# Kernel optimization log

Hardware: AMD Instinct MI355X
Metric: run time of the kernel (lower is better)

## Reference

```python
import jax, jax.numpy as jnp
import numpy as np

B = 2; QD = 128; H = QD; W = QD; NQ = QD * QD
EMBED = 256; HEADS = 8; POINTS = 4; D = EMBED // HEADS; FFN = 512


def setup_inputs() -> dict:
    key = jax.random.key(0)
    ks = jax.random.split(key, 16)
    s = 0.02
    rn = lambda k, shp: jax.random.normal(k, shp, jnp.float32) * s
    return {
        'q': jax.random.normal(ks[0], (B, NQ, EMBED), jnp.float32),
        'W_off': rn(ks[1], (EMBED, HEADS * POINTS * 2)),
        'b_off': rn(ks[2], (HEADS * POINTS * 2,)),
        'W_attn': rn(ks[3], (EMBED, HEADS * POINTS)),
        'b_attn': rn(ks[4], (HEADS * POINTS,)),
        'W_val': rn(ks[5], (EMBED, EMBED)),
        'b_val': rn(ks[6], (EMBED,)),
        'W_out': rn(ks[7], (EMBED, EMBED)),
        'b_out': rn(ks[8], (EMBED,)),
        'W1': rn(ks[9], (EMBED, FFN)),
        'b1': rn(ks[10], (FFN,)),
        'W2': rn(ks[11], (FFN, EMBED)),
        'b2': rn(ks[12], (EMBED,)),
        'gamma': jnp.ones((EMBED,), jnp.float32),
        'beta': jnp.zeros((EMBED,), jnp.float32),
    }


def _layernorm(x, g, b):
    m = x.mean(-1, keepdims=True)
    v = ((x - m) ** 2).mean(-1, keepdims=True)
    return (x - m) * jax.lax.rsqrt(v + 1e-5) * g + b


def _msda(q, W_off, b_off, W_attn, b_attn, W_val, b_val, W_out, b_out):
    # value projection; value == query here. (B, NQ, EMBED)
    value = q @ W_val + b_val
    v = value.reshape(B, NQ, HEADS, D).transpose(0, 2, 1, 3)  # (B, heads, Nv, D)

    off = (q @ W_off + b_off).reshape(B, NQ, HEADS, POINTS, 2)
    aw = jax.nn.softmax((q @ W_attn + b_attn).reshape(B, NQ, HEADS, POINTS), axis=-1)

    # reference points: torch.meshgrid(linspace, linspace, indexing='xy')
    lin = jnp.linspace(0.0, 1.0, QD)
    gx, gy = jnp.meshgrid(lin, lin, indexing='xy')
    ref = jnp.stack([gx, gy], -1).reshape(1, NQ, 1, 1, 2)

    # offset_normalizer = [W, H]; sampling locations in [0,1]
    loc = ref + off / jnp.array([W, H], jnp.float32)
    # grid_sample bilinear, align_corners=False: pixel = loc * size - 0.5
    px = (loc[..., 0] * W - 0.5).transpose(0, 2, 1, 3)  # (B, heads, NQ, P)
    py = (loc[..., 1] * H - 0.5).transpose(0, 2, 1, 3)

    x0 = jnp.floor(px)
    y0 = jnp.floor(py)
    sampled = jnp.zeros((B, HEADS, NQ, POINTS, D), jnp.float32)
    for dy in (0.0, 1.0):
        for dx in (0.0, 1.0):
            xi = x0 + dx
            yi = y0 + dy
            wgt = (1.0 - jnp.abs(px - xi)) * (1.0 - jnp.abs(py - yi))
            valid = ((xi >= 0) & (xi <= W - 1) & (yi >= 0) & (yi <= H - 1)).astype(jnp.float32)
            idx = (jnp.clip(yi, 0, H - 1).astype(jnp.int32) * W
                   + jnp.clip(xi, 0, W - 1).astype(jnp.int32))  # (B, heads, NQ, P)
            g = jnp.take_along_axis(v, idx.reshape(B, HEADS, NQ * POINTS, 1), axis=2)
            g = g.reshape(B, HEADS, NQ, POINTS, D)
            sampled = sampled + g * (wgt * valid)[..., None]

    awt = aw.transpose(0, 2, 1, 3)  # (B, heads, NQ, P)
    out = (sampled * awt[..., None]).sum(3)  # (B, heads, NQ, D)
    out = out.transpose(0, 2, 1, 3).reshape(B, NQ, EMBED)
    # mmcv: dropout(output_proj(out)) + identity ; dropout is identity at eval
    return out @ W_out + b_out + q


def reference(q, W_off, b_off, W_attn, b_attn, W_val, b_val, W_out, b_out,
              W1, b1, W2, b2, gamma, beta):
    attn = _msda(q, W_off, b_off, W_attn, b_attn, W_val, b_val, W_out, b_out)
    x = attn + q  # outer residual in the module (in addition to mmcv's internal one)
    ffn = _layernorm(jax.nn.relu(x @ W1 + b1) @ W2 + b2, gamma, beta)
    return x + ffn
```

## Files before the change

### kernel.cpp

```cpp
#include <hip/hip_runtime.h>
#include <hip/hip_bf16.h>
#include <cstddef>
#include <cstdint>

#define B_      2
#define QD_     128
#define NQ_     (QD_ * QD_)
#define EMBED_  256
#define HEADS_  8
#define POINTS_ 4
#define FFN_    512
#define RTOT_   (B_ * NQ_)
#define NCATP_  384

using bf16x8 = __attribute__((ext_vector_type(8))) short;
using f32x4  = __attribute__((ext_vector_type(4))) float;

__device__ __forceinline__ short f2bf(float f) {
    unsigned u = __float_as_uint(f);
    u += 0x7FFFu + ((u >> 16) & 1u);
    return (short)(u >> 16);
}
__device__ __forceinline__ float bf2f(short s) {
    return __uint_as_float(((unsigned)(unsigned short)s) << 16);
}

#define WCAT_ELEMS  (NCATP_ * 256)
#define WOUT_ELEMS  (256 * 256)
#define W1_ELEMS    (512 * 256)
#define W2_ELEMS    (256 * 512)
#define PREP_TOTAL  (WCAT_ELEMS + WOUT_ELEMS + W1_ELEMS + W2_ELEMS)
#define CVT_BLOCKS  (RTOT_ * EMBED_ / 8 / 256)
#define PREP_BLOCKS ((PREP_TOTAL + 255) / 256)

__global__ __launch_bounds__(256) void prep_all(
        const float* __restrict__ q, short* __restrict__ qbf,
        const float* __restrict__ Wv, const float* __restrict__ Wo,
        const float* __restrict__ Wa, const float* __restrict__ bv,
        const float* __restrict__ bo, const float* __restrict__ ba,
        const float* __restrict__ W_out, const float* __restrict__ W1,
        const float* __restrict__ W2,
        short* __restrict__ WcatT, short* __restrict__ WoutT,
        short* __restrict__ W1T, short* __restrict__ W2T,
        float* __restrict__ bcat) {
    const int b = blockIdx.x;
    if (b < CVT_BLOCKS) {
        const size_t i = (size_t)b * 256 + threadIdx.x;
        const float4 f0 = *(const float4*)(q + i * 8);
        const float4 f1 = *(const float4*)(q + i * 8 + 4);
        bf16x8 v;
        v[0] = f2bf(f0.x); v[1] = f2bf(f0.y); v[2] = f2bf(f0.z); v[3] = f2bf(f0.w);
        v[4] = f2bf(f1.x); v[5] = f2bf(f1.y); v[6] = f2bf(f1.z); v[7] = f2bf(f1.w);
        *(bf16x8*)(qbf + i * 8) = v;
        return;
    }
    int idx = (b - CVT_BLOCKS) * 256 + threadIdx.x;
    if (idx < WCAT_ELEMS) {
        int c = idx >> 8, k = idx & 255;
        float v = 0.f;
        if (c < 256)      v = Wv[k * 256 + c];
        else if (c < 320) v = Wo[k * 64 + (c - 256)];
        else if (c < 352) v = Wa[k * 32 + (c - 320)];
        WcatT[idx] = f2bf(v);
    } else if (idx < WCAT_ELEMS + WOUT_ELEMS) {
        int j = idx - WCAT_ELEMS; int c = j >> 8, k = j & 255;
        WoutT[j] = f2bf(W_out[k * 256 + c]);
    } else if (idx < WCAT_ELEMS + WOUT_ELEMS + W1_ELEMS) {
        int j = idx - (WCAT_ELEMS + WOUT_ELEMS); int c = j >> 8, k = j & 255;
        W1T[j] = f2bf(W1[k * 512 + c]);
    } else if (idx < PREP_TOTAL) {
        int j = idx - (WCAT_ELEMS + WOUT_ELEMS + W1_ELEMS); int c = j >> 9, k = j & 511;
        W2T[j] = f2bf(W2[k * 256 + c]);
    }
    if (idx < NCATP_) {
        float v = 0.f;
        if (idx < 256)      v = bv[idx];
        else if (idx < 320) v = bo[idx - 256];
        else if (idx < 352) v = ba[idx - 320];
        bcat[idx] = v;
    }
}

enum { EP_RELU_BF16 = 1, EP_ADD2Q_BF16 = 2, EP_SPLIT = 3 };

template <int EP>
__global__ __launch_bounds__(256) void gemm_mfma(
        const short* __restrict__ A,
        const short* __restrict__ Bt,
        const float* __restrict__ bias,
        const short* __restrict__ extra,
        float* __restrict__ Cf,
        short* __restrict__ Cb,
        int M, int N, int K) {
    __shared__ __align__(16) short As[2][128 * 64];
    __shared__ __align__(16) short Bs[2][128 * 64];

    const int t    = threadIdx.x;
    const int ln   = t & 63;
    const int w    = t >> 6;
    const int wr   = w >> 1;
    const int wc   = w & 1;
    const int lrow = ln & 15;
    const int lkg  = ln >> 4;

    const int gx   = gridDim.x;
    const int nwg  = gx * gridDim.y;
    const int flat = blockIdx.y * gx + blockIdx.x;
    const int q8   = nwg >> 3;
    const int swz  = (flat & 7) * q8 + (flat >> 3);
    const int row0 = (swz / gx) * 128;
    const int col0 = (swz % gx) * 128;

    f32x4 acc[4][4] = {};

    auto stage = [&](int buf, int k0) {
        #pragma unroll
        for (int j = 0; j < 4; ++j) {
            const int c0 = (w * 4 + j) * 64;
            const int c  = c0 + ln;
            const int r  = c >> 3;
            const int s  = (c & 7) ^ (r & 7);
            const short* ga = A  + (size_t)(row0 + r) * K + (k0 + s * 8);
            const short* gb = Bt + (size_t)(col0 + r) * K + (k0 + s * 8);
            __builtin_amdgcn_global_load_lds(
                (const __attribute__((address_space(1))) void*)ga,
                (__attribute__((address_space(3))) void*)&As[buf][c0 * 8], 16, 0, 0);
            __builtin_amdgcn_global_load_lds(
                (const __attribute__((address_space(1))) void*)gb,
                (__attribute__((address_space(3))) void*)&Bs[buf][c0 * 8], 16, 0, 0);
        }
    };

    stage(0, 0);
    __syncthreads();
    int cur = 0;
    for (int k0 = 0; k0 < K; k0 += 64) {
        if (k0 + 64 < K) stage(cur ^ 1, k0 + 64);
        #pragma unroll
        for (int ks = 0; ks < 2; ++ks) {
            const int slot = ((ks * 4 + lkg) ^ (lrow & 7)) * 8;
            bf16x8 af[4], bfr[4];
            #pragma unroll
            for (int m = 0; m < 4; ++m)
                af[m] = *(const bf16x8*)&As[cur][(wr * 64 + m * 16 + lrow) * 64 + slot];
            #pragma unroll
            for (int n = 0; n < 4; ++n)
                bfr[n] = *(const bf16x8*)&Bs[cur][(wc * 64 + n * 16 + lrow) * 64 + slot];
            #pragma unroll
            for (int m = 0; m < 4; ++m)
                #pragma unroll
                for (int n = 0; n < 4; ++n)
                    acc[m][n] = __builtin_amdgcn_mfma_f32_16x16x32_bf16(
                        af[m], bfr[n], acc[m][n], 0, 0, 0);
        }
        __syncthreads();
        cur ^= 1;
    }

    const int orow = (ln >> 4) * 4;
    const int ocol = ln & 15;
    #pragma unroll
    for (int m = 0; m < 4; ++m) {
        #pragma unroll
        for (int n = 0; n < 4; ++n) {
            const int col = col0 + wc * 64 + n * 16 + ocol;
            const float bv = bias[col];
            #pragma unroll
            for (int rr = 0; rr < 4; ++rr) {
                const int row = row0 + wr * 64 + m * 16 + orow + rr;
                float v = acc[m][n][rr] + bv;
                if (EP == EP_SPLIT) {
                    if (col < 256) Cb[(size_t)row * 256 + col] = f2bf(v);
                    else           Cf[(size_t)row * 128 + (col - 256)] = v;
                } else if (EP == EP_RELU_BF16) {
                    Cb[(size_t)row * N + col] = f2bf(fmaxf(v, 0.f));
                } else if (EP == EP_ADD2Q_BF16) {
                    v += 2.f * bf2f(extra[(size_t)row * N + col]);
                    Cb[(size_t)row * N + col] = f2bf(v);
                }
            }
        }
    }
}

__global__ __launch_bounds__(512) void gemm_ln(
        const short* __restrict__ A,
        const short* __restrict__ Bt,
        const float* __restrict__ bias,
        const short* __restrict__ xres,
        const float* __restrict__ gamma, const float* __restrict__ beta,
        float* __restrict__ out, int M, int K) {
    __shared__ __align__(16) short As[2][128 * 64];
    __shared__ __align__(16) short Bs[2][256 * 64];
    __shared__ float red[128][4][2];

    const int t    = threadIdx.x;
    const int ln   = t & 63;
    const int w    = t >> 6;
    const int wr   = w >> 2;
    const int wc   = w & 3;
    const int lrow = ln & 15;
    const int lkg  = ln >> 4;
    const int row0 = blockIdx.x * 128;

    f32x4 acc[4][4] = {};

    auto stage = [&](int buf, int k0) {
        #pragma unroll
        for (int j = 0; j < 2; ++j) {
            const int c0 = (w * 2 + j) * 64;
            const int c  = c0 + ln;
            const int r  = c >> 3;
            const int s  = (c & 7) ^ (r & 7);
            const short* ga = A + (size_t)(row0 + r) * K + (k0 + s * 8);
            __builtin_amdgcn_global_load_lds(
                (const __attribute__((address_space(1))) void*)ga,
                (__attribute__((address_space(3))) void*)&As[buf][c0 * 8], 16, 0, 0);
        }
        #pragma unroll
        for (int j = 0; j < 4; ++j) {
            const int c0 = (w * 4 + j) * 64;
            const int c  = c0 + ln;
            const int r  = c >> 3;
            const int s  = (c & 7) ^ (r & 7);
            const short* gb = Bt + (size_t)r * K + (k0 + s * 8);
            __builtin_amdgcn_global_load_lds(
                (const __attribute__((address_space(1))) void*)gb,
                (__attribute__((address_space(3))) void*)&Bs[buf][c0 * 8], 16, 0, 0);
        }
    };

    stage(0, 0);
    __syncthreads();
    int cur = 0;
    for (int k0 = 0; k0 < K; k0 += 64) {
        if (k0 + 64 < K) stage(cur ^ 1, k0 + 64);
        #pragma unroll
        for (int ks = 0; ks < 2; ++ks) {
            const int slot = ((ks * 4 + lkg) ^ (lrow & 7)) * 8;
            bf16x8 af[4], bfr[4];
            #pragma unroll
            for (int m = 0; m < 4; ++m)
                af[m] = *(const bf16x8*)&As[cur][(wr * 64 + m * 16 + lrow) * 64 + slot];
            #pragma unroll
            for (int n = 0; n < 4; ++n)
                bfr[n] = *(const bf16x8*)&Bs[cur][(wc * 64 + n * 16 + lrow) * 64 + slot];
            #pragma unroll
            for (int m = 0; m < 4; ++m)
                #pragma unroll
                for (int n = 0; n < 4; ++n)
                    acc[m][n] = __builtin_amdgcn_mfma_f32_16x16x32_bf16(
                        af[m], bfr[n], acc[m][n], 0, 0, 0);
        }
        __syncthreads();
        cur ^= 1;
    }

    const int orow = (ln >> 4) * 4;
    const int ocol = ln & 15;

    #pragma unroll
    for (int n = 0; n < 4; ++n) {
        const float bv = bias[wc * 64 + n * 16 + ocol];
        #pragma unroll
        for (int m = 0; m < 4; ++m)
            #pragma unroll
            for (int rr = 0; rr < 4; ++rr)
                acc[m][n][rr] += bv;
    }

    #pragma unroll
    for (int m = 0; m < 4; ++m) {
        #pragma unroll
        for (int rr = 0; rr < 4; ++rr) {
            float s = 0.f, sq = 0.f;
            #pragma unroll
            for (int n = 0; n < 4; ++n) {
                const float v = acc[m][n][rr];
                s += v; sq += v * v;
            }
            #pragma unroll
            for (int o = 1; o < 16; o <<= 1) {
                s  += __shfl_xor(s, o, 64);
                sq += __shfl_xor(sq, o, 64);
            }
            if (ocol == 0) {
                const int row = wr * 64 + m * 16 + orow + rr;
                red[row][wc][0] = s;
                red[row][wc][1] = sq;
            }
        }
    }
    __syncthreads();

    #pragma unroll
    for (int m = 0; m < 4; ++m) {
        #pragma unroll
        for (int rr = 0; rr < 4; ++rr) {
            const int row = wr * 64 + m * 16 + orow + rr;
            const float S  = red[row][0][0] + red[row][1][0] + red[row][2][0] + red[row][3][0];
            const float SQ = red[row][0][1] + red[row][1][1] + red[row][2][1] + red[row][3][1];
            const float mean = S * (1.0f / 256.0f);
            const float var  = SQ * (1.0f / 256.0f) - mean * mean;
            const float rs   = rsqrtf(var + 1e-5f);
            const size_t rbase = (size_t)(row0 + row) * 256;
            #pragma unroll
            for (int n = 0; n < 4; ++n) {
                const int col = wc * 64 + n * 16 + ocol;
                out[rbase + col] = bf2f(xres[rbase + col])
                                 + (acc[m][n][rr] - mean) * rs * gamma[col] + beta[col];
            }
        }
    }
}

__global__ __launch_bounds__(256) void msda_sample(
        const float* __restrict__ pm, const short* __restrict__ vcomp,
        short* __restrict__ msda) {
    __shared__ int   s_off[8][32][4];
    __shared__ float s_c[8][32][4];

    const int t  = threadIdx.x;
    const int r0 = blockIdx.x * 8;
    const int bq = r0 >> 14;

    {
        const int g = t >> 5, cmb = t & 31, h = cmb >> 2, p = cmb & 3;
        const int r = r0 + g;
        const int n = r & (NQ_ - 1);
        const int gi = n >> 7, gj = n & 127;
        const float* pr = pm + (size_t)r * 128;

        const float l0 = pr[64 + h * 4 + 0], l1 = pr[64 + h * 4 + 1];
        const float l2 = pr[64 + h * 4 + 2], l3 = pr[64 + h * 4 + 3];
        const float mx = fmaxf(fmaxf(l0, l1), fmaxf(l2, l3));
        const float sum = expf(l0 - mx) + expf(l1 - mx) + expf(l2 - mx) + expf(l3 - mx);
        const float lp = pr[64 + h * 4 + p];
        const float aw = expf(lp - mx) / sum;

        const float ox = pr[h * 8 + p * 2 + 0];
        const float oy = pr[h * 8 + p * 2 + 1];
        const float px = (gj * (1.0f / 127.0f) + ox * (1.0f / 128.0f)) * 128.0f - 0.5f;
        const float py = (gi * (1.0f / 127.0f) + oy * (1.0f / 128.0f)) * 128.0f - 0.5f;
        const float x0f = floorf(px), y0f = floorf(py);
        const int   x0 = (int)x0f, y0 = (int)y0f;
        const float fx = px - x0f, fy = py - y0f;
        const int x0c = min(max(x0, 0), 127), x1c = min(max(x0 + 1, 0), 127);
        const int y0c = min(max(y0, 0), 127), y1c = min(max(y0 + 1, 0), 127);
        const float vx0 = ((unsigned)x0 <= 127u) ? 1.f : 0.f;
        const float vx1 = ((unsigned)(x0 + 1) <= 127u) ? 1.f : 0.f;
        const float vy0 = ((unsigned)y0 <= 127u) ? 1.f : 0.f;
        const float vy1 = ((unsigned)(y0 + 1) <= 127u) ? 1.f : 0.f;

        s_off[g][cmb][0] = (y0c * 128 + x0c) * 512;
        s_off[g][cmb][1] = (y0c * 128 + x1c) * 512;
        s_off[g][cmb][2] = (y1c * 128 + x0c) * 512;
        s_off[g][cmb][3] = (y1c * 128 + x1c) * 512;
        s_c[g][cmb][0] = aw * (1.f - fx) * (1.f - fy) * vx0 * vy0;
        s_c[g][cmb][1] = aw * fx * (1.f - fy) * vx1 * vy0;
        s_c[g][cmb][2] = aw * (1.f - fx) * fy * vx0 * vy1;
        s_c[g][cmb][3] = aw * fx * fy * vx1 * vy1;
    }
    __syncthreads();

    const int half = t >> 7;
    const int h    = (t >> 4) & 7;
    const int dd   = t & 15;
    const char* vb = (const char*)vcomp + ((size_t)bq * NQ_ * 256 + h * 32 + dd * 2) * 2;

    #pragma unroll
    for (int it = 0; it < 4; ++it) {
        const int g = it * 2 + half;
        float a0 = 0.f, a1 = 0.f;
        #pragma unroll
        for (int p = 0; p < 4; ++p) {
            const int cmb = h * 4 + p;
            #pragma unroll
            for (int k = 0; k < 4; ++k) {
                const unsigned u = *(const unsigned*)(vb + s_off[g][cmb][k]);
                const float c = s_c[g][cmb][k];
                a0 += c * __uint_as_float(u << 16);
                a1 += c * __uint_as_float(u & 0xffff0000u);
            }
        }
        const int r = r0 + g;
        const unsigned o = (unsigned)(unsigned short)f2bf(a0)
                         | ((unsigned)(unsigned short)f2bf(a1) << 16);
        *(unsigned*)&msda[(size_t)r * 256 + h * 32 + dd * 2] = o;
    }
}

extern "C" void kernel_launch(void* const* d_in, const int* in_sizes, int n_in,
                              void* d_out, int out_size, void* d_ws, size_t ws_size,
                              hipStream_t stream) {
    const float* q      = (const float*)d_in[0];
    const float* b_out  = (const float*)d_in[8];
    const float* b1     = (const float*)d_in[10];
    const float* b2     = (const float*)d_in[12];
    const float* gamma  = (const float*)d_in[13];
    const float* beta   = (const float*)d_in[14];

    float* out = (float*)d_out;

    char* w = (char*)d_ws;
    float* pm    = (float*)w; w += (size_t)RTOT_ * 128 * 4;
    short* vcomp = (short*)w; w += (size_t)RTOT_ * 256 * 2;
    short* qbf   = (short*)w; w += (size_t)RTOT_ * EMBED_ * 2;
    short* msda  = (short*)w; w += (size_t)RTOT_ * EMBED_ * 2;
    short* xbf   = (short*)w; w += (size_t)RTOT_ * EMBED_ * 2;
    short* hid   = (short*)w; w += (size_t)RTOT_ * FFN_ * 2;
    short* WcatT = (short*)w; w += WCAT_ELEMS * 2;
    short* WoutT = (short*)w; w += WOUT_ELEMS * 2;
    short* W1T   = (short*)w; w += W1_ELEMS * 2;
    short* W2T   = (short*)w; w += W2_ELEMS * 2;
    float* bcat  = (float*)w; w += NCATP_ * 4;

    prep_all<<<CVT_BLOCKS + PREP_BLOCKS, 256, 0, stream>>>(
        q, qbf,
        (const float*)d_in[5], (const float*)d_in[1], (const float*)d_in[3],
        (const float*)d_in[6], (const float*)d_in[2], (const float*)d_in[4],
        (const float*)d_in[7], (const float*)d_in[9], (const float*)d_in[11],
        WcatT, WoutT, W1T, W2T, bcat);

    gemm_mfma<EP_SPLIT><<<dim3(NCATP_ / 128, RTOT_ / 128), 256, 0, stream>>>(
        qbf, WcatT, bcat, nullptr, pm, vcomp, RTOT_, NCATP_, EMBED_);

    msda_sample<<<RTOT_ / 8, 256, 0, stream>>>(pm, vcomp, msda);

    gemm_mfma<EP_ADD2Q_BF16><<<dim3(EMBED_ / 128, RTOT_ / 128), 256, 0, stream>>>(
        msda, WoutT, b_out, qbf, nullptr, xbf, RTOT_, EMBED_, EMBED_);

    gemm_mfma<EP_RELU_BF16><<<dim3(FFN_ / 128, RTOT_ / 128), 256, 0, stream>>>(
        xbf, W1T, b1, nullptr, nullptr, hid, RTOT_, FFN_, EMBED_);

    gemm_ln<<<RTOT_ / 128, 512, 0, stream>>>(
        hid, W2T, b2, xbf, gamma, beta, out, RTOT_, FFN_);
}
```

Before: 106.7 us.

## Fuse FFN up-projection, ReLU, down-projection and LayerNorm into one kernel

```diff
diff --git a/kernel.cpp b/kernel.cpp
--- a/kernel.cpp
+++ b/kernel.cpp
@@ -24,6 +24,10 @@
 __device__ __forceinline__ float bf2f(short s) {
     return __uint_as_float(((unsigned)(unsigned short)s) << 16);
 }
+
+#define GLDS(gp, lp) __builtin_amdgcn_global_load_lds( \
+        (const __attribute__((address_space(1))) void*)(gp), \
+        (__attribute__((address_space(3))) void*)(lp), 16, 0, 0)
 
 #define WCAT_ELEMS  (NCATP_ * 256)
 #define WOUT_ELEMS  (256 * 256)
@@ -81,7 +85,7 @@
     }
 }
 
-enum { EP_RELU_BF16 = 1, EP_ADD2Q_BF16 = 2, EP_SPLIT = 3 };
+enum { EP_ADD2Q_BF16 = 2, EP_SPLIT = 3 };
 
 template <int EP>
 __global__ __launch_bounds__(256) void gemm_mfma(
@@ -120,14 +124,8 @@
             const int c  = c0 + ln;
             const int r  = c >> 3;
             const int s  = (c & 7) ^ (r & 7);
-            const short* ga = A  + (size_t)(row0 + r) * K + (k0 + s * 8);
-            const short* gb = Bt + (size_t)(col0 + r) * K + (k0 + s * 8);
-            __builtin_amdgcn_global_load_lds(
-                (const __attribute__((address_space(1))) void*)ga,
-                (__attribute__((address_space(3))) void*)&As[buf][c0 * 8], 16, 0, 0);
-            __builtin_amdgcn_global_load_lds(
-                (const __attribute__((address_space(1))) void*)gb,
-                (__attribute__((address_space(3))) void*)&Bs[buf][c0 * 8], 16, 0, 0);
+            GLDS(A  + (size_t)(row0 + r) * K + (k0 + s * 8), &As[buf][c0 * 8]);
+            GLDS(Bt + (size_t)(col0 + r) * K + (k0 + s * 8), &Bs[buf][c0 * 8]);
         }
     };
 
@@ -172,8 +170,6 @@
                 if (EP == EP_SPLIT) {
                     if (col < 256) Cb[(size_t)row * 256 + col] = f2bf(v);
                     else           Cf[(size_t)row * 128 + (col - 256)] = v;
-                } else if (EP == EP_RELU_BF16) {
-                    Cb[(size_t)row * N + col] = f2bf(fmaxf(v, 0.f));
                 } else if (EP == EP_ADD2Q_BF16) {
                     v += 2.f * bf2f(extra[(size_t)row * N + col]);
                     Cb[(size_t)row * N + col] = f2bf(v);
@@ -183,15 +179,18 @@
     }
 }
 
-__global__ __launch_bounds__(512) void gemm_ln(
-        const short* __restrict__ A,
-        const short* __restrict__ Bt,
-        const float* __restrict__ bias,
-        const short* __restrict__ xres,
+__global__ __launch_bounds__(512) void ffn_ln(
+        const short* __restrict__ xbf,
+        const short* __restrict__ W1T,
+        const float* __restrict__ b1,
+        const short* __restrict__ W2T,
+        const float* __restrict__ b2,
         const float* __restrict__ gamma, const float* __restrict__ beta,
-        float* __restrict__ out, int M, int K) {
-    __shared__ __align__(16) short As[2][128 * 64];
-    __shared__ __align__(16) short Bs[2][256 * 64];
+        float* __restrict__ out) {
+    __shared__ __align__(16) short xs[4 * 128 * 64];
+    __shared__ __align__(16) short hl[128 * 64];
+    __shared__ __align__(16) short wb[2 * 128 * 64];
+    __shared__ __align__(16) short w2b[256 * 64];
     __shared__ float red[128][4][2];
 
     const int t    = threadIdx.x;
@@ -203,70 +202,129 @@
     const int lkg  = ln >> 4;
     const int row0 = blockIdx.x * 128;
 
-    f32x4 acc[4][4] = {};
-
-    auto stage = [&](int buf, int k0) {
+    auto stage_x = [&]() {
+        #pragma unroll
+        for (int j = 0; j < 8; ++j) {
+            const int c0 = (w * 8 + j) * 64;
+            const int cc = c0 + ln;
+            const int kt = cc >> 10, rem = cc & 1023;
+            const int r = rem >> 3;
+            const int s = (rem & 7) ^ (r & 7);
+            GLDS(xbf + (size_t)(row0 + r) * 256 + kt * 64 + s * 8, &xs[c0 * 8]);
+        }
+    };
+    auto stage_w1 = [&](int c, int kt, int buf) {
         #pragma unroll
         for (int j = 0; j < 2; ++j) {
             const int c0 = (w * 2 + j) * 64;
-            const int c  = c0 + ln;
-            const int r  = c >> 3;
-            const int s  = (c & 7) ^ (r & 7);
-            const short* ga = A + (size_t)(row0 + r) * K + (k0 + s * 8);
-            __builtin_amdgcn_global_load_lds(
-                (const __attribute__((address_space(1))) void*)ga,
-                (__attribute__((address_space(3))) void*)&As[buf][c0 * 8], 16, 0, 0);
-        }
+            const int cc = c0 + ln;
+            const int r = cc >> 3;
+            const int s = (cc & 7) ^ (r & 7);
+            GLDS(W1T + (size_t)(c * 128 + r) * 256 + kt * 64 + s * 8,
+                 &wb[buf * 8192 + c0 * 8]);
+        }
+    };
+    auto stage_w2 = [&](int c, int kt2) {
         #pragma unroll
         for (int j = 0; j < 4; ++j) {
             const int c0 = (w * 4 + j) * 64;
-            const int c  = c0 + ln;
-            const int r  = c >> 3;
-            const int s  = (c & 7) ^ (r & 7);
-            const short* gb = Bt + (size_t)r * K + (k0 + s * 8);
-            __builtin_amdgcn_global_load_lds(
-                (const __attribute__((address_space(1))) void*)gb,
-                (__attribute__((address_space(3))) void*)&Bs[buf][c0 * 8], 16, 0, 0);
+            const int cc = c0 + ln;
+            const int r = cc >> 3;
+            const int s = (cc & 7) ^ (r & 7);
+            GLDS(W2T + (size_t)r * 512 + c * 128 + kt2 * 64 + s * 8,
+                 &w2b[c0 * 8]);
         }
     };
 
-    stage(0, 0);
+    f32x4 acc2[4][4] = {};
+
+    stage_x();
+    stage_w1(0, 0, 0);
     __syncthreads();
-    int cur = 0;
-    for (int k0 = 0; k0 < K; k0 += 64) {
-        if (k0 + 64 < K) stage(cur ^ 1, k0 + 64);
-        #pragma unroll
-        for (int ks = 0; ks < 2; ++ks) {
-            const int slot = ((ks * 4 + lkg) ^ (lrow & 7)) * 8;
-            bf16x8 af[4], bfr[4];
-            #pragma unroll
-            for (int m = 0; m < 4; ++m)
-                af[m] = *(const bf16x8*)&As[cur][(wr * 64 + m * 16 + lrow) * 64 + slot];
-            #pragma unroll
-            for (int n = 0; n < 4; ++n)
-                bfr[n] = *(const bf16x8*)&Bs[cur][(wc * 64 + n * 16 + lrow) * 64 + slot];
-            #pragma unroll
-            for (int m = 0; m < 4; ++m)
+
+    #pragma unroll 1
+    for (int c = 0; c < 4; ++c) {
+        f32x4 acc1[4][2] = {};
+        int buf = 0;
+        #pragma unroll
+        for (int kt = 0; kt < 4; ++kt) {
+            if (kt < 3) {
+                stage_w1(c, kt + 1, buf ^ 1);
+            } else {
+                stage_w2(c, 0);
+                if (c < 3) stage_w1(c + 1, 0, 0);
+            }
+            #pragma unroll
+            for (int ks = 0; ks < 2; ++ks) {
+                const int slot = ((ks * 4 + lkg) ^ (lrow & 7)) * 8;
+                bf16x8 af[4], bfr[2];
+                #pragma unroll
+                for (int m = 0; m < 4; ++m)
+                    af[m] = *(const bf16x8*)&xs[kt * 8192 + (wr * 64 + m * 16 + lrow) * 64 + slot];
+                #pragma unroll
+                for (int n = 0; n < 2; ++n)
+                    bfr[n] = *(const bf16x8*)&wb[buf * 8192 + (wc * 32 + n * 16 + lrow) * 64 + slot];
+                #pragma unroll
+                for (int m = 0; m < 4; ++m)
+                    #pragma unroll
+                    for (int n = 0; n < 2; ++n)
+                        acc1[m][n] = __builtin_amdgcn_mfma_f32_16x16x32_bf16(
+                            af[m], bfr[n], acc1[m][n], 0, 0, 0);
+            }
+            __syncthreads();
+            buf ^= 1;
+        }
+
+        #pragma unroll
+        for (int half = 0; half < 2; ++half) {
+            if (half == 1) stage_w2(c, 1);
+            if ((wc >> 1) == half) {
+                #pragma unroll
+                for (int n = 0; n < 2; ++n) {
+                    const int kk = (wc & 1) * 32 + n * 16 + lrow;
+                    const float bv = b1[c * 128 + half * 64 + kk];
+                    #pragma unroll
+                    for (int m = 0; m < 4; ++m)
+                        #pragma unroll
+                        for (int rr = 0; rr < 4; ++rr) {
+                            const int row = wr * 64 + m * 16 + lkg * 4 + rr;
+                            const float v = fmaxf(acc1[m][n][rr] + bv, 0.f);
+                            hl[row * 64 + ((kk >> 3) ^ (row & 7)) * 8 + (kk & 7)] = f2bf(v);
+                        }
+                }
+            }
+            __syncthreads();
+            #pragma unroll
+            for (int ks = 0; ks < 2; ++ks) {
+                const int slot = ((ks * 4 + lkg) ^ (lrow & 7)) * 8;
+                bf16x8 af[4], bfr[4];
+                #pragma unroll
+                for (int m = 0; m < 4; ++m)
+                    af[m] = *(const bf16x8*)&hl[(wr * 64 + m * 16 + lrow) * 64 + slot];
                 #pragma unroll
                 for (int n = 0; n < 4; ++n)
-                    acc[m][n] = __builtin_amdgcn_mfma_f32_16x16x32_bf16(
-                        af[m], bfr[n], acc[m][n], 0, 0, 0);
-        }
-        __syncthreads();
-        cur ^= 1;
-    }
-
-    const int orow = (ln >> 4) * 4;
-    const int ocol = ln & 15;
-
+                    bfr[n] = *(const bf16x8*)&w2b[(wc * 64 + n * 16 + lrow) * 64 + slot];
+                #pragma unroll
+                for (int m = 0; m < 4; ++m)
+                    #pragma unroll
+                    for (int n = 0; n < 4; ++n)
+                        acc2[m][n] = __builtin_amdgcn_mfma_f32_16x16x32_bf16(
+                            af[m], bfr[n], acc2[m][n], 0, 0, 0);
+            }
+            __syncthreads();
+        }
+    }
+
+    const int orow = lkg * 4;
+    const int ocol = lrow;
     #pragma unroll
     for (int n = 0; n < 4; ++n) {
-        const float bv = bias[wc * 64 + n * 16 + ocol];
+        const float bv = b2[wc * 64 + n * 16 + ocol];
         #pragma unroll
         for (int m = 0; m < 4; ++m)
             #pragma unroll
             for (int rr = 0; rr < 4; ++rr)
-                acc[m][n][rr] += bv;
+                acc2[m][n][rr] += bv;
     }
 
     #pragma unroll
@@ -276,7 +334,7 @@
             float s = 0.f, sq = 0.f;
             #pragma unroll
             for (int n = 0; n < 4; ++n) {
-                const float v = acc[m][n][rr];
+                const float v = acc2[m][n][rr];
                 s += v; sq += v * v;
             }
             #pragma unroll
@@ -307,8 +365,10 @@
             #pragma unroll
             for (int n = 0; n < 4; ++n) {
                 const int col = wc * 64 + n * 16 + ocol;
-                out[rbase + col] = bf2f(xres[rbase + col])
-                                 + (acc[m][n][rr] - mean) * rs * gamma[col] + beta[col];
+                const int kk  = n * 16 + ocol;
+                const float xv = bf2f(xs[wc * 8192 + row * 64 +
+                                         ((kk >> 3) ^ (row & 7)) * 8 + (kk & 7)]);
+                out[rbase + col] = xv + (acc2[m][n][rr] - mean) * rs * gamma[col] + beta[col];
             }
         }
     }
@@ -408,7 +468,6 @@
     short* qbf   = (short*)w; w += (size_t)RTOT_ * EMBED_ * 2;
     short* msda  = (short*)w; w += (size_t)RTOT_ * EMBED_ * 2;
     short* xbf   = (short*)w; w += (size_t)RTOT_ * EMBED_ * 2;
-    short* hid   = (short*)w; w += (size_t)RTOT_ * FFN_ * 2;
     short* WcatT = (short*)w; w += WCAT_ELEMS * 2;
     short* WoutT = (short*)w; w += WOUT_ELEMS * 2;
     short* W1T   = (short*)w; w += W1_ELEMS * 2;
@@ -430,9 +489,6 @@
     gemm_mfma<EP_ADD2Q_BF16><<<dim3(EMBED_ / 128, RTOT_ / 128), 256, 0, stream>>>(
         msda, WoutT, b_out, qbf, nullptr, xbf, RTOT_, EMBED_, EMBED_);
 
-    gemm_mfma<EP_RELU_BF16><<<dim3(FFN_ / 128, RTOT_ / 128), 256, 0, stream>>>(
-        xbf, W1T, b1, nullptr, nullptr, hid, RTOT_, FFN_, EMBED_);
-
-    gemm_ln<<<RTOT_ / 128, 512, 0, stream>>>(
-        hid, W2T, b2, xbf, gamma, beta, out, RTOT_, FFN_);
-}
+    ffn_ln<<<RTOT_ / 128, 512, 0, stream>>>(
+        xbf, W1T, b1, W2T, b2, gamma, beta, out);
+}
```

Result: no change. 104.6 us (-1.9%).

## Shrink gemm_ln row tile to 64 with single-buffered B staging

Applied to the files above, without the earlier changes.

```diff
diff --git a/kernel.cpp b/kernel.cpp
--- a/kernel.cpp
+++ b/kernel.cpp
@@ -24,6 +24,10 @@
 __device__ __forceinline__ float bf2f(short s) {
     return __uint_as_float(((unsigned)(unsigned short)s) << 16);
 }
+
+#define GLDS(gp, lp) __builtin_amdgcn_global_load_lds( \
+        (const __attribute__((address_space(1))) void*)(gp), \
+        (__attribute__((address_space(3))) void*)(lp), 16, 0, 0)
 
 #define WCAT_ELEMS  (NCATP_ * 256)
 #define WOUT_ELEMS  (256 * 256)
@@ -120,14 +124,8 @@
             const int c  = c0 + ln;
             const int r  = c >> 3;
             const int s  = (c & 7) ^ (r & 7);
-            const short* ga = A  + (size_t)(row0 + r) * K + (k0 + s * 8);
-            const short* gb = Bt + (size_t)(col0 + r) * K + (k0 + s * 8);
-            __builtin_amdgcn_global_load_lds(
-                (const __attribute__((address_space(1))) void*)ga,
-                (__attribute__((address_space(3))) void*)&As[buf][c0 * 8], 16, 0, 0);
-            __builtin_amdgcn_global_load_lds(
-                (const __attribute__((address_space(1))) void*)gb,
-                (__attribute__((address_space(3))) void*)&Bs[buf][c0 * 8], 16, 0, 0);
+            GLDS(A  + (size_t)(row0 + r) * K + (k0 + s * 8), &As[buf][c0 * 8]);
+            GLDS(Bt + (size_t)(col0 + r) * K + (k0 + s * 8), &Bs[buf][c0 * 8]);
         }
     };
 
@@ -183,68 +181,63 @@
     }
 }
 
-__global__ __launch_bounds__(512) void gemm_ln(
+__global__ __launch_bounds__(256) void gemm_ln(
         const short* __restrict__ A,
         const short* __restrict__ Bt,
         const float* __restrict__ bias,
         const short* __restrict__ xres,
         const float* __restrict__ gamma, const float* __restrict__ beta,
         float* __restrict__ out, int M, int K) {
-    __shared__ __align__(16) short As[2][128 * 64];
-    __shared__ __align__(16) short Bs[2][256 * 64];
-    __shared__ float red[128][4][2];
+    __shared__ __align__(16) short As[2][64 * 64];
+    __shared__ __align__(16) short Bs[256 * 64];
+    __shared__ float red[64][4][2];
 
     const int t    = threadIdx.x;
     const int ln   = t & 63;
     const int w    = t >> 6;
-    const int wr   = w >> 2;
-    const int wc   = w & 3;
     const int lrow = ln & 15;
     const int lkg  = ln >> 4;
-    const int row0 = blockIdx.x * 128;
+    const int row0 = blockIdx.x * 64;
 
     f32x4 acc[4][4] = {};
 
-    auto stage = [&](int buf, int k0) {
+    auto stage_a = [&](int buf, int k0) {
         #pragma unroll
         for (int j = 0; j < 2; ++j) {
             const int c0 = (w * 2 + j) * 64;
             const int c  = c0 + ln;
             const int r  = c >> 3;
             const int s  = (c & 7) ^ (r & 7);
-            const short* ga = A + (size_t)(row0 + r) * K + (k0 + s * 8);
-            __builtin_amdgcn_global_load_lds(
-                (const __attribute__((address_space(1))) void*)ga,
-                (__attribute__((address_space(3))) void*)&As[buf][c0 * 8], 16, 0, 0);
-        }
-        #pragma unroll
-        for (int j = 0; j < 4; ++j) {
-            const int c0 = (w * 4 + j) * 64;
+            GLDS(A + (size_t)(row0 + r) * K + (k0 + s * 8), &As[buf][c0 * 8]);
+        }
+    };
+    auto stage_b = [&](int k0) {
+        #pragma unroll
+        for (int j = 0; j < 8; ++j) {
+            const int c0 = (w * 8 + j) * 64;
             const int c  = c0 + ln;
             const int r  = c >> 3;
             const int s  = (c & 7) ^ (r & 7);
-            const short* gb = Bt + (size_t)r * K + (k0 + s * 8);
-            __builtin_amdgcn_global_load_lds(
-                (const __attribute__((address_space(1))) void*)gb,
-                (__attribute__((address_space(3))) void*)&Bs[buf][c0 * 8], 16, 0, 0);
+            GLDS(Bt + (size_t)r * K + (k0 + s * 8), &Bs[c0 * 8]);
         }
     };
 
-    stage(0, 0);
+    stage_a(0, 0);
+    stage_b(0);
     __syncthreads();
-    int cur = 0;
-    for (int k0 = 0; k0 < K; k0 += 64) {
-        if (k0 + 64 < K) stage(cur ^ 1, k0 + 64);
+    int buf = 0;
+    for (int kt = 0; kt < 8; ++kt) {
+        if (kt < 7) stage_a(buf ^ 1, kt * 64 + 64);
         #pragma unroll
         for (int ks = 0; ks < 2; ++ks) {
             const int slot = ((ks * 4 + lkg) ^ (lrow & 7)) * 8;
             bf16x8 af[4], bfr[4];
             #pragma unroll
             for (int m = 0; m < 4; ++m)
-                af[m] = *(const bf16x8*)&As[cur][(wr * 64 + m * 16 + lrow) * 64 + slot];
+                af[m] = *(const bf16x8*)&As[buf][(m * 16 + lrow) * 64 + slot];
             #pragma unroll
             for (int n = 0; n < 4; ++n)
-                bfr[n] = *(const bf16x8*)&Bs[cur][(wc * 64 + n * 16 + lrow) * 64 + slot];
+                bfr[n] = *(const bf16x8*)&Bs[(w * 64 + n * 16 + lrow) * 64 + slot];
             #pragma unroll
             for (int m = 0; m < 4; ++m)
                 #pragma unroll
@@ -253,15 +246,19 @@
                         af[m], bfr[n], acc[m][n], 0, 0, 0);
         }
         __syncthreads();
-        cur ^= 1;
-    }
-
-    const int orow = (ln >> 4) * 4;
-    const int ocol = ln & 15;
+        if (kt < 7) {
+            stage_b(kt * 64 + 64);
+            __syncthreads();
+        }
+        buf ^= 1;
+    }
+
+    const int orow = lkg * 4;
+    const int ocol = lrow;
 
     #pragma unroll
     for (int n = 0; n < 4; ++n) {
-        const float bv = bias[wc * 64 + n * 16 + ocol];
+        const float bv = bias[w * 64 + n * 16 + ocol];
         #pragma unroll
         for (int m = 0; m < 4; ++m)
             #pragma unroll
@@ -285,9 +282,9 @@
                 sq += __shfl_xor(sq, o, 64);
             }
             if (ocol == 0) {
-                const int row = wr * 64 + m * 16 + orow + rr;
-                red[row][wc][0] = s;
-                red[row][wc][1] = sq;
+                const int row = m * 16 + orow + rr;
+                red[row][w][0] = s;
+                red[row][w][1] = sq;
             }
         }
     }
@@ -297,7 +294,7 @@
     for (int m = 0; m < 4; ++m) {
         #pragma unroll
         for (int rr = 0; rr < 4; ++rr) {
-            const int row = wr * 64 + m * 16 + orow + rr;
+            const int row = m * 16 + orow + rr;
             const float S  = red[row][0][0] + red[row][1][0] + red[row][2][0] + red[row][3][0];
             const float SQ = red[row][0][1] + red[row][1][1] + red[row][2][1] + red[row][3][1];
             const float mean = S * (1.0f / 256.0f);
@@ -306,7 +303,7 @@
             const size_t rbase = (size_t)(row0 + row) * 256;
             #pragma unroll
             for (int n = 0; n < 4; ++n) {
-                const int col = wc * 64 + n * 16 + ocol;
+                const int col = w * 64 + n * 16 + ocol;
                 out[rbase + col] = bf2f(xres[rbase + col])
                                  + (acc[m][n][rr] - mean) * rs * gamma[col] + beta[col];
             }
@@ -433,6 +430,6 @@
     gemm_mfma<EP_RELU_BF16><<<dim3(FFN_ / 128, RTOT_ / 128), 256, 0, stream>>>(
         xbf, W1T, b1, nullptr, nullptr, hid, RTOT_, FFN_, EMBED_);
 
-    gemm_ln<<<RTOT_ / 128, 512, 0, stream>>>(
+    gemm_ln<<<RTOT_ / 64, 256, 0, stream>>>(
         hid, W2T, b2, xbf, gamma, beta, out, RTOT_, FFN_);
 }
```

New measurement: 105.9 us. No clear change (-0.7%).
